# Kernel optimization log

Hardware: AMD Instinct MI355X
Metric: run time of the kernel (lower is better)

## Reference

```python
import jax, jax.numpy as jnp
from jax import lax
import numpy as np

ALPHA = 0.5; EPS = 1e-6; RANK_PAIRS = 100
W_MEAN = 0.5; W_STD = 0.5
L_STAT = 1.0; L_RANK = 1.0; L_SMOOTH = 1.0
LABELS = np.array([5, 8, 13], dtype=np.int32)
TGT_CV = np.array([0.077, 0.227, 0.348], dtype=np.float32)


def _erode(mask_f):
    # torch: 1 - max_pool2d(1-x, k=3, pad=1); implicit -inf padding means
    # out-of-bounds pixels act as foreground -> min-pool with +inf init.
    return lax.reduce_window(mask_f, jnp.inf, lax.min, (3, 3), (1, 1), 'SAME') > 0.5


def _per_region(pred, pix, region, tgt_cv, key):
    # pred, pix: [H,W] float; region: [H,W] bool
    H, W = pred.shape
    HW = H * W
    regf = region.astype(jnp.float32)
    e1 = _erode(regf)
    e2 = _erode(e1.astype(jnp.float32))  # erode(region, iterations=2)
    core1 = jnp.where(jnp.sum(e1) < 2, region, e1)
    core2 = jnp.where(jnp.sum(e2) < 3, core1, e2)
    n_reg = jnp.sum(region)

    # ---- std (coefficient-of-variation) term on core2
    c2 = core2.astype(jnp.float32)
    n2 = jnp.sum(c2)
    n2s = jnp.maximum(n2, 1.0)
    mu = jnp.sum(pred * c2) / n2s
    var = jnp.sum(c2 * (pred - mu) ** 2) / n2s  # unbiased=False
    cv = jnp.sqrt(var) / (jnp.abs(mu) + EPS)
    std_val = jnp.abs(cv - tgt_cv)
    std_valid = (n_reg >= 3) & (n2 >= 3)

    # ---- pairwise rank term on core1 (sampled-pair path; realistic regions
    # always have n > full_pair_threshold=20)
    c1f = core1.reshape(-1).astype(jnp.float32)
    n1 = jnp.sum(c1f)
    p = jnp.where(n1 > 0, c1f / jnp.maximum(n1, 1.0), 1.0 / HW)
    k1, k2 = jax.random.split(key)
    ii = jax.random.choice(k1, HW, (RANK_PAIRS,), replace=True, p=p)
    jj = jax.random.choice(k2, HW, (RANK_PAIRS,), replace=True, p=p)
    pf = pred.reshape(-1)
    xf = pix.reshape(-1)
    s = jnp.sign(xf[ii] - xf[jj])
    pv = ((ii != jj) & (s != 0)).astype(jnp.float32)
    hinge = jax.nn.relu(-(pf[ii] - pf[jj]) * s)
    npv = jnp.sum(pv)
    rank_val = jnp.sum(hinge * pv) / jnp.maximum(npv, 1.0)
    rank_valid = (n_reg >= 2) & (n1 >= 2) & (npv > 0)

    # ---- smoothness term on core2
    dx = jnp.abs(pred[:, 1:] - pred[:, :-1])
    mx = (core2[:, 1:] & core2[:, :-1]).astype(jnp.float32)
    dy = jnp.abs(pred[1:, :] - pred[:-1, :])
    my = (core2[1:, :] & core2[:-1, :]).astype(jnp.float32)
    cx = jnp.sum(mx); cy = jnp.sum(my)
    mean_x = jnp.sum(dx * mx) / jnp.maximum(cx, 1.0)
    mean_y = jnp.sum(dy * my) / jnp.maximum(cy, 1.0)
    hx = (cx > 0).astype(jnp.float32); hy = (cy > 0).astype(jnp.float32)
    npres = hx + hy
    smooth_val = (mean_x * hx + mean_y * hy) / jnp.maximum(npres, 1.0)
    smooth_valid = (n_reg >= 3) & (n2 >= 3) & (npres > 0)

    return std_val, std_valid, rank_val, rank_valid, smooth_val, smooth_valid


def _masked_mean(v, valid):
    vf = valid.astype(jnp.float32)
    c = jnp.sum(vf)
    return jnp.where(c > 0, jnp.sum(v * vf) / jnp.maximum(c, 1.0), 0.0)


def _forward(pred, target, lab14, img1, img2):
    B, _, H, W = pred.shape
    p2 = pred[:, 0]
    lab = lab14[:, 0]
    t1 = img1[:, 0]
    t2 = img2[:, 0]
    pix = (1.0 - ALPHA) * (1.0 - t1) + ALPHA * t2  # pixel_map
    loss_mean = jnp.mean(jnp.abs(pred - target))

    labels = jnp.asarray(LABELS)
    regions = lab[:, None, :, :] == labels[None, :, None, None]  # [B,3,H,W]
    R = regions.reshape(B * 3, H, W)
    P = jnp.broadcast_to(p2[:, None], (B, 3, H, W)).reshape(B * 3, H, W)
    X = jnp.broadcast_to(pix[:, None], (B, 3, H, W)).reshape(B * 3, H, W)
    T = jnp.tile(jnp.asarray(TGT_CV), B)  # [B*3], label-minor matches reshape
    keys = jax.random.split(jax.random.key(42), B * 3)

    sv, svd, rv, rvd, mv, mvd = jax.vmap(_per_region)(P, X, R, T, keys)
    loss_std = _masked_mean(sv, svd)
    loss_rank = _masked_mean(rv, rvd)
    loss_smooth = _masked_mean(mv, mvd)

    loss_stat = W_MEAN * loss_mean + W_STD * loss_std
    return L_STAT * loss_stat + L_RANK * loss_rank + L_SMOOTH * loss_smooth


def setup_inputs() -> dict:
    key = jax.random.key(0)
    k1, k2, k3, k4, k5 = jax.random.split(key, 5)
    B, H, W = 16, 512, 512
    pred = jax.random.normal(k1, (B, 1, H, W), dtype=jnp.float32)
    target = jax.random.normal(k2, (B, 1, H, W), dtype=jnp.float32)
    lab14 = jax.random.randint(k3, (B, 1, H, W), 0, 15, dtype=jnp.int32)
    img1 = jax.random.uniform(k4, (B, 1, H, W), dtype=jnp.float32)
    img2 = jax.random.uniform(k5, (B, 1, H, W), dtype=jnp.float32)
    return {"pred": pred, "target": target, "lab14": lab14, "img1": img1, "img2": img2}


def reference(pred, target, lab14, img1, img2):
    return _forward(pred, target, lab14, img1, img2)
```

## Files before the change

### kernel.cpp

```cpp
#include <hip/hip_runtime.h>

#define BB 16
#define HH 512
#define WW 512
#define BH 8
#define NR (BH+5)
#define NBANDS (HH/BH)
#define NREG 48
#define HWTOT (HH*WW)

#define OFF_SUMABS 4608
#define OFF_COUNTS 4616
#define OFF_RANKV  6344
#define OFF_RANKD  6536
#define OFF_MREG   8192
#define MASKBYTES  (48LL*512*8*8)
#define OFF_ME1    (OFF_MREG + MASKBYTES)

__device__ __forceinline__ unsigned int hashu(unsigned int x) {
  x ^= x >> 16; x *= 0x7feb352dU; x ^= x >> 15; x *= 0x846ca68bU; x ^= x >> 16;
  return x;
}

__global__ __launch_bounds__(256) void pass1_kernel(
    const float* __restrict__ pred, const float* __restrict__ target,
    const int* __restrict__ lab,
    double* __restrict__ sums, double* __restrict__ sumAbs,
    int* __restrict__ counts,
    unsigned long long* __restrict__ mRegG, unsigned long long* __restrict__ mE1G)
{
  __shared__ unsigned long long REG[3][NR][8];
  __shared__ unsigned long long Hh [3][NR][8];
  __shared__ unsigned long long E1v[3][NR][8];
  __shared__ unsigned long long E1H[3][NR][8];
  __shared__ unsigned long long E2v[3][NR][8];
  __shared__ int   Lc[27];
  __shared__ float RED[4][37];

  const int t    = threadIdx.x;
  const int lane = t & 63;
  const int wv   = t >> 6;
  const int r0   = blockIdx.x * BH;
  const int b    = blockIdx.y;
  const int R    = r0 - 3;

  if (t < 27) Lc[t] = 0;

  for (int lr = 0; lr < NR; ++lr) {
    int gy = R + lr;
    int l1 = -1, l2 = -1;
    if ((unsigned)gy < (unsigned)HH) {
      const int* lp = lab + ((size_t)b*HH + gy)*WW;
      l1 = lp[t]; l2 = lp[t+256];
    }
    unsigned long long m1, m2;
    m1 = __ballot(l1 == 5);  m2 = __ballot(l2 == 5);
    if (lane == 0) { REG[0][lr][wv] = m1; REG[0][lr][wv+4] = m2; }
    m1 = __ballot(l1 == 8);  m2 = __ballot(l2 == 8);
    if (lane == 0) { REG[1][lr][wv] = m1; REG[1][lr][wv+4] = m2; }
    m1 = __ballot(l1 == 13); m2 = __ballot(l2 == 13);
    if (lane == 0) { REG[2][lr][wv] = m1; REG[2][lr][wv+4] = m2; }
  }
  __syncthreads();

  for (int task = t; task < 3*NR*8; task += 256) {
    int w = task & 7, q = task >> 3;
    int lr = q % NR, li = q / NR;
    unsigned long long m  = REG[li][lr][w];
    unsigned long long lm = (m << 1) | (w ? (REG[li][lr][w-1] >> 63) : 1ULL);
    unsigned long long rm = (m >> 1) | ((w < 7) ? (REG[li][lr][w+1] << 63) : (1ULL << 63));
    Hh[li][lr][w] = m & lm & rm;
  }
  __syncthreads();
  for (int task = t; task < 3*(NR-2)*8; task += 256) {
    int w = task & 7, q = task >> 3;
    int lr = q % (NR-2) + 1, li = q / (NR-2);
    int gy = R + lr;
    unsigned long long v = Hh[li][lr][w];
    if (gy - 1 >= 0) v &= Hh[li][lr-1][w];
    if (gy + 1 < HH) v &= Hh[li][lr+1][w];
    E1v[li][lr][w] = v;
  }
  __syncthreads();
  for (int task = t; task < 3*(NR-2)*8; task += 256) {
    int w = task & 7, q = task >> 3;
    int lr = q % (NR-2) + 1, li = q / (NR-2);
    unsigned long long m  = E1v[li][lr][w];
    unsigned long long lm = (m << 1) | (w ? (E1v[li][lr][w-1] >> 63) : 1ULL);
    unsigned long long rm = (m >> 1) | ((w < 7) ? (E1v[li][lr][w+1] << 63) : (1ULL << 63));
    E1H[li][lr][w] = m & lm & rm;
  }
  __syncthreads();
  for (int task = t; task < 3*(NR-4)*8; task += 256) {
    int w = task & 7, q = task >> 3;
    int lr = q % (NR-4) + 2, li = q / (NR-4);
    int gy = R + lr;
    unsigned long long v = E1H[li][lr][w];
    if (gy - 1 >= 0) v &= E1H[li][lr-1][w];
    if (gy + 1 < HH) v &= E1H[li][lr+1][w];
    E2v[li][lr][w] = v;
  }
  __syncthreads();

  for (int task = t; task < 3*BH*8; task += 256) {
    int w   = task & 7;
    int row = (task >> 3) % BH;
    int li  = task / (BH*8);
    int gy  = r0 + row;
    int lr  = row + 3;
    size_t base = (((size_t)(b*3 + li))*HH + gy)*8 + w;
    mRegG[base] = REG[li][lr][w];
    mE1G[base]  = E1v[li][lr][w];
  }

  for (int task = t; task < 9*64; task += 256) {
    int idx = task & 63, combo = task >> 6;
    int li = combo / 3, m = combo % 3;
    int row = idx >> 3, w = idx & 7;
    int lr = row + 3, gy = r0 + row;
    const unsigned long long (*M)[8] = (m == 0) ? REG[li] : ((m == 1) ? E1v[li] : E2v[li]);
    unsigned long long mm = M[lr][w];
    int c = __popcll(mm);
    unsigned long long nx = (w < 7) ? M[lr][w+1] : 0ULL;
    int cx = __popcll(mm & ((mm >> 1) | (nx << 63)));
    int cy = (gy > 0) ? __popcll(mm & M[lr-1][w]) : 0;
    atomicAdd(&Lc[combo*3 + 0], c);
    atomicAdd(&Lc[combo*3 + 1], cx);
    atomicAdd(&Lc[combo*3 + 2], cy);
  }

  float aP[9]  = {};
  float aP2[9] = {};
  float aDX[9] = {};
  float aDY[9] = {};
  float aAbs = 0.f;

  const int w1 = wv;
  const int b1 = lane;

  float p1_prev = 0.f, p2_prev = 0.f;
  if (r0 > 0) {
    const float* pr = pred + ((size_t)b*HH + (r0-1))*WW;
    p1_prev = pr[t]; p2_prev = pr[t+256];
  }

  __syncthreads();

  if (t < 27) {
    int combo = t / 3, stat = t % 3;
    int li = combo / 3, m = combo % 3;
    atomicAdd(counts + (b*3 + li)*9 + stat*3 + m, Lc[t]);
  }

  unsigned int ub1 = 0, ub2 = 0;
  #pragma unroll
  for (int li = 0; li < 3; ++li) {
    #pragma unroll
    for (int m = 0; m < 3; ++m) {
      const int cb = li*3 + m;
      const unsigned long long (*M)[8] = (m == 0) ? REG[li] : ((m == 1) ? E1v[li] : E2v[li]);
      ub1 |= (((unsigned int)(M[2][w1]   >> b1)) & 1u) << cb;
      ub2 |= (((unsigned int)(M[2][w1+4] >> b1)) & 1u) << cb;
    }
  }

  const bool hasR2 = (t < 255);
  for (int row = 0; row < BH; ++row) {
    int gy = r0 + row;
    int lr = row + 3;
    const float* prow = pred   + ((size_t)b*HH + gy)*WW;
    const float* trow = target + ((size_t)b*HH + gy)*WW;
    float p1 = prow[t], p2 = prow[t+256];
    float pr1 = prow[t+1];
    float pr2 = hasR2 ? prow[t+257] : 0.f;
    float tg1 = trow[t], tg2 = trow[t+256];
    aAbs += fabsf(p1 - tg1) + fabsf(p2 - tg2);
    float d1 = fabsf(pr1 - p1);
    float d2 = fabsf(pr2 - p2);
    float v1 = fabsf(p1 - p1_prev);
    float v2 = fabsf(p2 - p2_prev);
    float p1s = p1*p1, p2s = p2*p2;
    const bool hasUp = (gy > 0);
    unsigned int nb1 = 0, nb2 = 0;
    #pragma unroll
    for (int li = 0; li < 3; ++li) {
      #pragma unroll
      for (int m = 0; m < 3; ++m) {
        const int cb = li*3 + m;
        const unsigned long long (*M)[8] = (m == 0) ? REG[li] : ((m == 1) ? E1v[li] : E2v[li]);
        unsigned long long cur1 = M[lr][w1];
        unsigned long long cur2 = M[lr][w1+4];
        unsigned int c1 = (unsigned int)(cur1 >> b1) & 1u;
        unsigned int c2 = (unsigned int)(cur2 >> b1) & 1u;
        unsigned int r1, r2;
        if (b1 < 63) {
          r1 = (unsigned int)(cur1 >> (b1+1)) & 1u;
          r2 = (unsigned int)(cur2 >> (b1+1)) & 1u;
        } else {
          r1 = (unsigned int)M[lr][w1+1] & 1u;
          r2 = (w1 < 3) ? ((unsigned int)M[lr][w1+5] & 1u) : 0u;
        }
        unsigned int u1 = hasUp ? ((ub1 >> cb) & 1u) : 0u;
        unsigned int u2 = hasUp ? ((ub2 >> cb) & 1u) : 0u;
        if (c1) { aP[cb] += p1; aP2[cb] += p1s; }
        if (c2) { aP[cb] += p2; aP2[cb] += p2s; }
        if (c1 & r1) aDX[cb] += d1;
        if (hasR2 & (bool)(c2 & r2)) aDX[cb] += d2;
        if (c1 & u1) aDY[cb] += v1;
        if (c2 & u2) aDY[cb] += v2;
        nb1 |= c1 << cb;
        nb2 |= c2 << cb;
      }
    }
    ub1 = nb1; ub2 = nb2;
    p1_prev = p1; p2_prev = p2;
  }

  #pragma unroll
  for (int cb = 0; cb < 9; ++cb) {
    float s0 = aP[cb], s1 = aP2[cb], s2 = aDX[cb], s3 = aDY[cb];
    for (int off = 32; off; off >>= 1) {
      s0 += __shfl_down(s0, off);
      s1 += __shfl_down(s1, off);
      s2 += __shfl_down(s2, off);
      s3 += __shfl_down(s3, off);
    }
    if (lane == 0) {
      RED[wv][0*9 + cb] = s0;
      RED[wv][1*9 + cb] = s1;
      RED[wv][2*9 + cb] = s2;
      RED[wv][3*9 + cb] = s3;
    }
  }
  {
    float va = aAbs;
    for (int off = 32; off; off >>= 1) va += __shfl_down(va, off);
    if (lane == 0) RED[wv][36] = va;
  }
  __syncthreads();
  if (t < 37) {
    float s = RED[0][t] + RED[1][t] + RED[2][t] + RED[3][t];
    if (t < 36) {
      int stat = t / 9, cb = t % 9;
      int li = cb / 3, m = cb % 3;
      atomicAdd(sums + (size_t)(b*3 + li)*12 + stat*3 + m, (double)s);
    } else {
      atomicAdd(sumAbs, (double)s);
    }
  }
}

__global__ __launch_bounds__(256) void pass2_kernel(
    const float* __restrict__ pred, const float* __restrict__ img1,
    const float* __restrict__ img2,
    const unsigned long long* __restrict__ mRegG,
    const unsigned long long* __restrict__ mE1G,
    const int* __restrict__ counts,
    float* __restrict__ rankval, int* __restrict__ rankvalid)
{
  const int r = blockIdx.x;
  const int b = r / 3;
  const int t = threadIdx.x;
  __shared__ int rowc[HH];
  __shared__ int pre[HH];
  __shared__ int grpPre[64];
  __shared__ int idxArr[200];
  __shared__ float redH[100];
  __shared__ int   redP[100];

  int n_reg = counts[r*9 + 0];
  int n_e1  = counts[r*9 + 1];
  int useE1 = (n_e1 >= 2);
  int n1 = useE1 ? n_e1 : n_reg;
  if (!(n_reg >= 2 && n1 >= 2)) {
    if (t == 0) { rankval[r] = 0.f; rankvalid[r] = 0; }
    return;
  }
  const unsigned long long* M = (useE1 ? mE1G : mRegG) + (size_t)r*HH*8;

  {
    int row = t*2;
    int c0 = 0, c1 = 0;
    #pragma unroll
    for (int w = 0; w < 8; ++w) c0 += __popcll(M[row*8 + w]);
    #pragma unroll
    for (int w = 0; w < 8; ++w) c1 += __popcll(M[(row+1)*8 + w]);
    rowc[row] = c0; rowc[row+1] = c1;
  }
  __syncthreads();
  if (t < 64) {
    int base = t*8, s = 0;
    #pragma unroll
    for (int k = 0; k < 8; ++k) s += rowc[base + k];
    int v = s;
    for (int off = 1; off < 64; off <<= 1) {
      int o = __shfl_up(v, off);
      if (t >= off) v += o;
    }
    grpPre[t] = v - s;
  }
  __syncthreads();
  if (t < 64) {
    int s = grpPre[t];
    int base = t*8;
    #pragma unroll
    for (int k = 0; k < 8; ++k) { pre[base + k] = s; s += rowc[base + k]; }
  }
  __syncthreads();

  if (t < 200) {
    unsigned int h = hashu(0x9e3779b9u + (unsigned)(r*200 + t));
    float u = (float)(h >> 8) * (1.0f / 16777216.0f);
    int k = (int)(u * (float)n1);
    if (k >= n1) k = n1 - 1;
    if (k < 0) k = 0;
    int lo = 0, hi = HH;
    while (hi - lo > 1) { int mid = (lo + hi) >> 1; if (pre[mid] <= k) lo = mid; else hi = mid; }
    int row = lo;
    int local = k - pre[row];
    int idx = 0;
    #pragma unroll
    for (int w = 0; w < 8; ++w) {
      unsigned long long mm = M[row*8 + w];
      int c = __popcll(mm);
      if (local < c) {
        for (int i = 0; i < local; ++i) mm &= mm - 1;
        idx = row*WW + w*64 + __builtin_ctzll(mm);
        local = 1 << 20;
      } else {
        local -= c;
      }
    }
    idxArr[t] = idx;
  }
  __syncthreads();

  if (t < 100) {
    int ii = idxArr[t], jj = idxArr[t+100];
    size_t base = (size_t)b * HWTOT;
    float pi = pred[base+ii], pj = pred[base+jj];
    float xi = 0.5f*(1.f - img1[base+ii]) + 0.5f*img2[base+ii];
    float xj = 0.5f*(1.f - img1[base+jj]) + 0.5f*img2[base+jj];
    float s = (xi > xj) ? 1.f : ((xi < xj) ? -1.f : 0.f);
    int pv = (ii != jj) && (s != 0.f);
    float hinge = fmaxf(0.f, -(pi - pj)*s);
    redH[t] = pv ? hinge : 0.f;
    redP[t] = pv;
  }
  __syncthreads();
  if (t == 0) {
    float sh = 0.f; int sp = 0;
    for (int i = 0; i < 100; ++i) { sh += redH[i]; sp += redP[i]; }
    rankval[r]   = sh / (float)(sp > 0 ? sp : 1);
    rankvalid[r] = (sp > 0) ? 1 : 0;
  }
}

__global__ __launch_bounds__(64) void pass3_kernel(
    const double* __restrict__ sums, const double* __restrict__ sumAbs,
    const int* __restrict__ counts,
    const float* __restrict__ rankval, const int* __restrict__ rankvalid,
    float* __restrict__ out)
{
  const int t = threadIdx.x;
  __shared__ double svv[NREG]; __shared__ int svd[NREG];
  __shared__ double smv[NREG]; __shared__ int smd[NREG];
  if (t < NREG) {
    int li = t % 3;
    const int* C = counts + t*9;
    const double* S = sums + (size_t)t*12;
    int n_reg = C[0], n_e1 = C[1], n_e2 = C[2];
    int m1 = (n_e1 < 2) ? 0 : 1;
    int m2 = (n_e2 < 3) ? m1 : 2;
    int n2 = C[m2];
    double n2s = (double)(n2 > 1 ? n2 : 1);
    double mu  = S[m2] / n2s;
    double var = S[3+m2] / n2s - mu*mu;
    if (var < 0.0) var = 0.0;
    double cv = sqrt(var) / (fabs(mu) + 1e-6);
    double tcv = (li == 0) ? 0.077 : ((li == 1) ? 0.227 : 0.348);
    svv[t] = fabs(cv - tcv);
    svd[t] = (n_reg >= 3 && n2 >= 3);
    int cx = C[3+m2], cy = C[6+m2];
    double mean_x = S[6+m2] / (double)(cx > 1 ? cx : 1);
    double mean_y = S[9+m2] / (double)(cy > 1 ? cy : 1);
    int hx = (cx > 0), hy = (cy > 0);
    int npres = hx + hy;
    smv[t] = (mean_x*hx + mean_y*hy) / (double)(npres > 1 ? npres : 1);
    smd[t] = (n_reg >= 3 && n2 >= 3 && npres > 0);
  }
  __syncthreads();
  if (t == 0) {
    double s_std = 0, s_sm = 0, s_rk = 0;
    int c_std = 0, c_sm = 0, c_rk = 0;
    for (int i = 0; i < NREG; ++i) {
      if (svd[i])       { s_std += svv[i];     c_std++; }
      if (smd[i])       { s_sm  += smv[i];     c_sm++;  }
      if (rankvalid[i]) { s_rk  += rankval[i]; c_rk++;  }
    }
    double loss_std = c_std ? s_std / c_std : 0.0;
    double loss_sm  = c_sm  ? s_sm  / c_sm  : 0.0;
    double loss_rk  = c_rk  ? s_rk  / c_rk  : 0.0;
    double loss_mean = sumAbs[0] / (double)((long long)BB * HWTOT);
    double total = 0.5*loss_mean + 0.5*loss_std + loss_rk + loss_sm;
    out[0] = (float)total;
  }
}

extern "C" void kernel_launch(void* const* d_in, const int* in_sizes, int n_in,
                              void* d_out, int out_size, void* d_ws, size_t ws_size,
                              hipStream_t stream) {
  const float* pred   = (const float*)d_in[0];
  const float* target = (const float*)d_in[1];
  const int*   lab    = (const int*)d_in[2];
  const float* img1   = (const float*)d_in[3];
  const float* img2   = (const float*)d_in[4];
  float* out = (float*)d_out;
  char* ws = (char*)d_ws;

  double* sums    = (double*)ws;
  double* sumAbs  = (double*)(ws + OFF_SUMABS);
  int*    counts  = (int*)(ws + OFF_COUNTS);
  float*  rankval = (float*)(ws + OFF_RANKV);
  int*    rankvld = (int*)(ws + OFF_RANKD);
  unsigned long long* mReg = (unsigned long long*)(ws + OFF_MREG);
  unsigned long long* mE1  = (unsigned long long*)(ws + OFF_ME1);

  hipMemsetAsync(ws, 0, 8192, stream);

  dim3 g1(NBANDS, BB);
  pass1_kernel<<<g1, 256, 0, stream>>>(pred, target, lab, sums, sumAbs, counts, mReg, mE1);
  pass2_kernel<<<NREG, 256, 0, stream>>>(pred, img1, img2, mReg, mE1, counts, rankval, rankvld);
  pass3_kernel<<<1, 64, 0, stream>>>(sums, sumAbs, counts, rankval, rankvld, out);
}
```

Baseline: 160.1 us.

## Column-bitmask erosion in pass1, precomputed row counts, fuse final reduction into pass2

Pass1 now uses 512 threads, one per column, and a 16-row band. Each thread keeps a 21-bit vertical bitmask per label, and erosion becomes shift-ANDs plus neighbor exchange through shared memory, replacing the multi-stage shared-memory erosion of 64-bit row words. Pass1 also writes per-row popcounts, so pass2 no longer recomputes them from the masks. Pass2 reduces the rank hinge with warp shuffles. The old pass3 is folded into pass2 through a last-block atomic counter, which removes one kernel launch. The trade-offs are more registers per thread, 16-bit packed counters that could overflow in principle, and grid-level completion detection that relies on atomics and fences.

```diff
diff --git a/kernel.cpp b/kernel.cpp
--- a/kernel.cpp
+++ b/kernel.cpp
@@ -3,17 +3,21 @@
 #define BB 16
 #define HH 512
 #define WW 512
-#define BH 8
+#define BH 16
 #define NR (BH+5)
 #define NBANDS (HH/BH)
 #define NREG 48
 #define HWTOT (HH*WW)
+#define MASK21 0x1FFFFFu
 
 #define OFF_SUMABS 4608
 #define OFF_COUNTS 4616
 #define OFF_RANKV  6344
 #define OFF_RANKD  6536
-#define OFF_MREG   8192
+#define OFF_CTR    6728
+#define OFF_ROWCR  8192
+#define OFF_ROWCE  (OFF_ROWCR + 48*512*4)
+#define OFF_MREG   (OFF_ROWCE + 48*512*4)
 #define MASKBYTES  (48LL*512*8*8)
 #define OFF_ME1    (OFF_MREG + MASKBYTES)
 
@@ -22,198 +26,172 @@
   return x;
 }
 
-__global__ __launch_bounds__(256) void pass1_kernel(
+__global__ __launch_bounds__(512, 4) void pass1_kernel(
     const float* __restrict__ pred, const float* __restrict__ target,
     const int* __restrict__ lab,
     double* __restrict__ sums, double* __restrict__ sumAbs,
     int* __restrict__ counts,
-    unsigned long long* __restrict__ mRegG, unsigned long long* __restrict__ mE1G)
+    unsigned long long* __restrict__ mRegG, unsigned long long* __restrict__ mE1G,
+    int* __restrict__ rowcR, int* __restrict__ rowcE)
 {
-  __shared__ unsigned long long REG[3][NR][8];
-  __shared__ unsigned long long Hh [3][NR][8];
-  __shared__ unsigned long long E1v[3][NR][8];
-  __shared__ unsigned long long E1H[3][NR][8];
-  __shared__ unsigned long long E2v[3][NR][8];
-  __shared__ int   Lc[27];
-  __shared__ float RED[4][37];
+  __shared__ unsigned long long XCH[514];
+  __shared__ unsigned long long NB0[512];
+  __shared__ unsigned long long NB1[512];
+  __shared__ unsigned int      NB2[512];
+  __shared__ int   RC[96];
+  __shared__ float RED[8][37];
+  __shared__ unsigned int CNT[8][14];
 
   const int t    = threadIdx.x;
   const int lane = t & 63;
   const int wv   = t >> 6;
+  const int c    = t;
   const int r0   = blockIdx.x * BH;
   const int b    = blockIdx.y;
   const int R    = r0 - 3;
 
-  if (t < 27) Lc[t] = 0;
-
+  if (t < 96) RC[t] = 0;
+
+  unsigned int OOR = 0;
+  {
+    int topClip = -R;
+    if (topClip > 0) OOR |= (1u << topClip) - 1u;
+    int botStart = HH - R;
+    if (botStart < NR) OOR |= (~0u << botStart) & ((1u << NR) - 1u);
+  }
+
+  unsigned int colm0 = 0, colm1 = 0, colm2 = 0;
   for (int lr = 0; lr < NR; ++lr) {
     int gy = R + lr;
-    int l1 = -1, l2 = -1;
     if ((unsigned)gy < (unsigned)HH) {
-      const int* lp = lab + ((size_t)b*HH + gy)*WW;
-      l1 = lp[t]; l2 = lp[t+256];
-    }
-    unsigned long long m1, m2;
-    m1 = __ballot(l1 == 5);  m2 = __ballot(l2 == 5);
-    if (lane == 0) { REG[0][lr][wv] = m1; REG[0][lr][wv+4] = m2; }
-    m1 = __ballot(l1 == 8);  m2 = __ballot(l2 == 8);
-    if (lane == 0) { REG[1][lr][wv] = m1; REG[1][lr][wv+4] = m2; }
-    m1 = __ballot(l1 == 13); m2 = __ballot(l2 == 13);
-    if (lane == 0) { REG[2][lr][wv] = m1; REG[2][lr][wv+4] = m2; }
-  }
-  __syncthreads();
-
-  for (int task = t; task < 3*NR*8; task += 256) {
-    int w = task & 7, q = task >> 3;
-    int lr = q % NR, li = q / NR;
-    unsigned long long m  = REG[li][lr][w];
-    unsigned long long lm = (m << 1) | (w ? (REG[li][lr][w-1] >> 63) : 1ULL);
-    unsigned long long rm = (m >> 1) | ((w < 7) ? (REG[li][lr][w+1] << 63) : (1ULL << 63));
-    Hh[li][lr][w] = m & lm & rm;
-  }
-  __syncthreads();
-  for (int task = t; task < 3*(NR-2)*8; task += 256) {
-    int w = task & 7, q = task >> 3;
-    int lr = q % (NR-2) + 1, li = q / (NR-2);
-    int gy = R + lr;
-    unsigned long long v = Hh[li][lr][w];
-    if (gy - 1 >= 0) v &= Hh[li][lr-1][w];
-    if (gy + 1 < HH) v &= Hh[li][lr+1][w];
-    E1v[li][lr][w] = v;
-  }
-  __syncthreads();
-  for (int task = t; task < 3*(NR-2)*8; task += 256) {
-    int w = task & 7, q = task >> 3;
-    int lr = q % (NR-2) + 1, li = q / (NR-2);
-    unsigned long long m  = E1v[li][lr][w];
-    unsigned long long lm = (m << 1) | (w ? (E1v[li][lr][w-1] >> 63) : 1ULL);
-    unsigned long long rm = (m >> 1) | ((w < 7) ? (E1v[li][lr][w+1] << 63) : (1ULL << 63));
-    E1H[li][lr][w] = m & lm & rm;
-  }
-  __syncthreads();
-  for (int task = t; task < 3*(NR-4)*8; task += 256) {
-    int w = task & 7, q = task >> 3;
-    int lr = q % (NR-4) + 2, li = q / (NR-4);
-    int gy = R + lr;
-    unsigned long long v = E1H[li][lr][w];
-    if (gy - 1 >= 0) v &= E1H[li][lr-1][w];
-    if (gy + 1 < HH) v &= E1H[li][lr+1][w];
-    E2v[li][lr][w] = v;
-  }
-  __syncthreads();
-
-  for (int task = t; task < 3*BH*8; task += 256) {
-    int w   = task & 7;
-    int row = (task >> 3) % BH;
-    int li  = task / (BH*8);
-    int gy  = r0 + row;
-    int lr  = row + 3;
-    size_t base = (((size_t)(b*3 + li))*HH + gy)*8 + w;
-    mRegG[base] = REG[li][lr][w];
-    mE1G[base]  = E1v[li][lr][w];
-  }
-
-  for (int task = t; task < 9*64; task += 256) {
-    int idx = task & 63, combo = task >> 6;
-    int li = combo / 3, m = combo % 3;
-    int row = idx >> 3, w = idx & 7;
-    int lr = row + 3, gy = r0 + row;
-    const unsigned long long (*M)[8] = (m == 0) ? REG[li] : ((m == 1) ? E1v[li] : E2v[li]);
-    unsigned long long mm = M[lr][w];
-    int c = __popcll(mm);
-    unsigned long long nx = (w < 7) ? M[lr][w+1] : 0ULL;
-    int cx = __popcll(mm & ((mm >> 1) | (nx << 63)));
-    int cy = (gy > 0) ? __popcll(mm & M[lr-1][w]) : 0;
-    atomicAdd(&Lc[combo*3 + 0], c);
-    atomicAdd(&Lc[combo*3 + 1], cx);
-    atomicAdd(&Lc[combo*3 + 2], cy);
-  }
-
-  float aP[9]  = {};
-  float aP2[9] = {};
-  float aDX[9] = {};
-  float aDY[9] = {};
-  float aAbs = 0.f;
-
-  const int w1 = wv;
-  const int b1 = lane;
-
-  float p1_prev = 0.f, p2_prev = 0.f;
-  if (r0 > 0) {
-    const float* pr = pred + ((size_t)b*HH + (r0-1))*WW;
-    p1_prev = pr[t]; p2_prev = pr[t+256];
-  }
-
-  __syncthreads();
-
-  if (t < 27) {
-    int combo = t / 3, stat = t % 3;
-    int li = combo / 3, m = combo % 3;
-    atomicAdd(counts + (b*3 + li)*9 + stat*3 + m, Lc[t]);
-  }
-
-  unsigned int ub1 = 0, ub2 = 0;
+      int l = lab[((size_t)b*HH + gy)*WW + c];
+      colm0 |= (l == 5)  ? (1u << lr) : 0u;
+      colm1 |= (l == 8)  ? (1u << lr) : 0u;
+      colm2 |= (l == 13) ? (1u << lr) : 0u;
+    }
+  }
+
+  unsigned long long pk =  (unsigned long long)(colm0 | OOR)
+        | ((unsigned long long)(colm1 | OOR) << 21)
+        | ((unsigned long long)(colm2 | OOR) << 42);
+  XCH[c+1] = pk;
+  if (t == 0) { XCH[0] = ~0ull; XCH[513] = ~0ull; }
+  __syncthreads();
+  unsigned long long hp = pk & XCH[c] & XCH[c+2];
+  unsigned int e1a[3];
   #pragma unroll
   for (int li = 0; li < 3; ++li) {
-    #pragma unroll
-    for (int m = 0; m < 3; ++m) {
-      const int cb = li*3 + m;
-      const unsigned long long (*M)[8] = (m == 0) ? REG[li] : ((m == 1) ? E1v[li] : E2v[li]);
-      ub1 |= (((unsigned int)(M[2][w1]   >> b1)) & 1u) << cb;
-      ub2 |= (((unsigned int)(M[2][w1+4] >> b1)) & 1u) << cb;
-    }
-  }
-
-  const bool hasR2 = (t < 255);
+    unsigned int h = (unsigned int)((hp >> (21*li)) & MASK21);
+    e1a[li] = h & (h >> 1) & (h << 1);
+  }
+  __syncthreads();
+  unsigned long long pk2 =  (unsigned long long)((e1a[0] | OOR) & MASK21)
+        | ((unsigned long long)((e1a[1] | OOR) & MASK21) << 21)
+        | ((unsigned long long)((e1a[2] | OOR) & MASK21) << 42);
+  XCH[c+1] = pk2;
+  __syncthreads();
+  unsigned long long hp2 = pk2 & XCH[c] & XCH[c+2];
+  unsigned int e2a[3];
+  #pragma unroll
+  for (int li = 0; li < 3; ++li) {
+    unsigned int h = (unsigned int)((hp2 >> (21*li)) & MASK21);
+    e2a[li] = h & (h >> 1) & (h << 1);
+  }
+
+  unsigned int mS[9] = { colm0, e1a[0], e2a[0],
+                         colm1, e1a[1], e2a[1],
+                         colm2, e1a[2], e2a[2] };
+
+  {
+    unsigned long long p0 = 0, p1 = 0;
+    #pragma unroll
+    for (int cb = 0; cb < 4; ++cb) p0 |= (unsigned long long)((mS[cb] >> 3) & 0xFFFFu) << (cb*16);
+    #pragma unroll
+    for (int cb = 4; cb < 8; ++cb) p1 |= (unsigned long long)((mS[cb] >> 3) & 0xFFFFu) << ((cb-4)*16);
+    NB0[c] = p0; NB1[c] = p1; NB2[c] = (mS[8] >> 3) & 0xFFFFu;
+  }
+  __syncthreads();
+  unsigned long long nb0 = (c < 511) ? NB0[c+1] : 0ull;
+  unsigned long long nb1 = (c < 511) ? NB1[c+1] : 0ull;
+  unsigned int       nb2 = (c < 511) ? NB2[c+1] : 0u;
+
+  {
+    unsigned int pkc[14];
+    #pragma unroll
+    for (int j = 0; j < 14; ++j) pkc[j] = 0;
+    #pragma unroll
+    for (int cb = 0; cb < 9; ++cb) {
+      unsigned int w16 = (mS[cb] >> 3) & 0xFFFFu;
+      unsigned int nbw;
+      if (cb < 4)      nbw = (unsigned int)(nb0 >> (cb*16)) & 0xFFFFu;
+      else if (cb < 8) nbw = (unsigned int)(nb1 >> ((cb-4)*16)) & 0xFFFFu;
+      else             nbw = nb2 & 0xFFFFu;
+      unsigned int mcl = mS[cb] & ~OOR;
+      unsigned int q   = mcl & (mcl << 1);
+      unsigned int cnt = __popc(w16);
+      unsigned int cx  = __popc(w16 & nbw);
+      unsigned int cy  = __popc((q >> 3) & 0xFFFFu);
+      int k0 = cb*3;
+      pkc[(k0  )>>1] |= cnt << (((k0  )&1)*16);
+      pkc[(k0+1)>>1] |= cx  << (((k0+1)&1)*16);
+      pkc[(k0+2)>>1] |= cy  << (((k0+2)&1)*16);
+    }
+    #pragma unroll
+    for (int j = 0; j < 14; ++j) {
+      unsigned int v = pkc[j];
+      for (int off = 32; off; off >>= 1) v += __shfl_down(v, off);
+      if (lane == 0) CNT[wv][j] = v;
+    }
+  }
+
   for (int row = 0; row < BH; ++row) {
-    int gy = r0 + row;
-    int lr = row + 3;
-    const float* prow = pred   + ((size_t)b*HH + gy)*WW;
-    const float* trow = target + ((size_t)b*HH + gy)*WW;
-    float p1 = prow[t], p2 = prow[t+256];
-    float pr1 = prow[t+1];
-    float pr2 = hasR2 ? prow[t+257] : 0.f;
-    float tg1 = trow[t], tg2 = trow[t+256];
-    aAbs += fabsf(p1 - tg1) + fabsf(p2 - tg2);
-    float d1 = fabsf(pr1 - p1);
-    float d2 = fabsf(pr2 - p2);
-    float v1 = fabsf(p1 - p1_prev);
-    float v2 = fabsf(p2 - p2_prev);
-    float p1s = p1*p1, p2s = p2*p2;
-    const bool hasUp = (gy > 0);
-    unsigned int nb1 = 0, nb2 = 0;
+    int lr = row + 3, gy = r0 + row;
     #pragma unroll
     for (int li = 0; li < 3; ++li) {
-      #pragma unroll
-      for (int m = 0; m < 3; ++m) {
-        const int cb = li*3 + m;
-        const unsigned long long (*M)[8] = (m == 0) ? REG[li] : ((m == 1) ? E1v[li] : E2v[li]);
-        unsigned long long cur1 = M[lr][w1];
-        unsigned long long cur2 = M[lr][w1+4];
-        unsigned int c1 = (unsigned int)(cur1 >> b1) & 1u;
-        unsigned int c2 = (unsigned int)(cur2 >> b1) & 1u;
-        unsigned int r1, r2;
-        if (b1 < 63) {
-          r1 = (unsigned int)(cur1 >> (b1+1)) & 1u;
-          r2 = (unsigned int)(cur2 >> (b1+1)) & 1u;
-        } else {
-          r1 = (unsigned int)M[lr][w1+1] & 1u;
-          r2 = (w1 < 3) ? ((unsigned int)M[lr][w1+5] & 1u) : 0u;
-        }
-        unsigned int u1 = hasUp ? ((ub1 >> cb) & 1u) : 0u;
-        unsigned int u2 = hasUp ? ((ub2 >> cb) & 1u) : 0u;
-        if (c1) { aP[cb] += p1; aP2[cb] += p1s; }
-        if (c2) { aP[cb] += p2; aP2[cb] += p2s; }
-        if (c1 & r1) aDX[cb] += d1;
-        if (hasR2 & (bool)(c2 & r2)) aDX[cb] += d2;
-        if (c1 & u1) aDY[cb] += v1;
-        if (c2 & u2) aDY[cb] += v2;
-        nb1 |= c1 << cb;
-        nb2 |= c2 << cb;
+      unsigned long long wR = __ballot((mS[li*3]   >> lr) & 1u);
+      unsigned long long wE = __ballot((mS[li*3+1] >> lr) & 1u);
+      if (lane == 0) {
+        size_t base = (((size_t)(b*3 + li))*HH + gy)*8 + wv;
+        mRegG[base] = wR; mE1G[base] = wE;
+        atomicAdd(&RC[     li*BH + row], (int)__popcll(wR));
+        atomicAdd(&RC[48 + li*BH + row], (int)__popcll(wE));
       }
     }
-    ub1 = nb1; ub2 = nb2;
-    p1_prev = p1; p2_prev = p2;
+  }
+
+  float aP[9] = {}, aP2[9] = {}, aDX[9] = {}, aDY[9] = {};
+  float aAbs = 0.f;
+  const float* pB = pred   + (size_t)b*HH*WW;
+  const float* tB = target + (size_t)b*HH*WW;
+  float p_prev = (r0 > 0) ? pB[(size_t)(r0-1)*WW + c] : 0.f;
+  const int cR = (c < 511) ? c + 1 : c;
+
+  #pragma unroll
+  for (int row = 0; row < BH; ++row) {
+    const int lr = row + 3, gy = r0 + row;
+    const float* prow = pB + (size_t)gy*WW;
+    float p  = prow[c];
+    float pr = prow[cR];
+    float tg = tB[(size_t)gy*WW + c];
+    aAbs += fabsf(p - tg);
+    float d = fabsf(pr - p);
+    float v = (gy > 0) ? fabsf(p - p_prev) : 0.f;
+    #pragma unroll
+    for (int cb = 0; cb < 9; ++cb) {
+      unsigned int cur = mS[cb];
+      unsigned int c1 = (cur >> lr) & 1u;
+      unsigned int u1 = (cur >> (lr-1)) & 1u;
+      unsigned int r1;
+      if (cb < 4)      r1 = (unsigned int)(nb0 >> (cb*16 + row)) & 1u;
+      else if (cb < 8) r1 = (unsigned int)(nb1 >> ((cb-4)*16 + row)) & 1u;
+      else             r1 = (nb2 >> row) & 1u;
+      float f = c1 ? p : 0.f;
+      aP[cb]  += f;
+      aP2[cb]  = fmaf(f, p, aP2[cb]);
+      aDX[cb] += (c1 & r1) ? d : 0.f;
+      aDY[cb] += (c1 & u1) ? v : 0.f;
+    }
+    p_prev = p;
   }
 
   #pragma unroll
@@ -226,10 +204,8 @@
       s3 += __shfl_down(s3, off);
     }
     if (lane == 0) {
-      RED[wv][0*9 + cb] = s0;
-      RED[wv][1*9 + cb] = s1;
-      RED[wv][2*9 + cb] = s2;
-      RED[wv][3*9 + cb] = s3;
+      RED[wv][0*9 + cb] = s0; RED[wv][1*9 + cb] = s1;
+      RED[wv][2*9 + cb] = s2; RED[wv][3*9 + cb] = s3;
     }
   }
   {
@@ -238,15 +214,38 @@
     if (lane == 0) RED[wv][36] = va;
   }
   __syncthreads();
+
   if (t < 37) {
-    float s = RED[0][t] + RED[1][t] + RED[2][t] + RED[3][t];
+    float s = 0.f;
+    #pragma unroll
+    for (int w = 0; w < 8; ++w) s += RED[w][t];
     if (t < 36) {
-      int stat = t / 9, cb = t % 9;
-      int li = cb / 3, m = cb % 3;
+      int stat = t / 9, cb = t % 9, li = cb / 3, m = cb % 3;
       atomicAdd(sums + (size_t)(b*3 + li)*12 + stat*3 + m, (double)s);
     } else {
       atomicAdd(sumAbs, (double)s);
     }
+  }
+  if (t < 14) {
+    unsigned int s = 0;
+    #pragma unroll
+    for (int w = 0; w < 8; ++w) s += CNT[w][t];
+    int k0 = t*2;
+    #pragma unroll
+    for (int h = 0; h < 2; ++h) {
+      int k = k0 + h;
+      if (k < 27) {
+        unsigned int val = (s >> (h*16)) & 0xFFFFu;
+        int cb = k / 3, stat = k % 3, li = cb / 3, m = cb % 3;
+        atomicAdd(counts + (b*3 + li)*9 + stat*3 + m, (int)val);
+      }
+    }
+  }
+  if (t < 96) {
+    int type = t / 48, rem = t % 48;
+    int li = rem / BH, row = rem % BH, gy = r0 + row;
+    int* dst = type ? rowcE : rowcR;
+    dst[((size_t)(b*3 + li))*HH + gy] = RC[t];
   }
 }
 
@@ -255,155 +254,166 @@
     const float* __restrict__ img2,
     const unsigned long long* __restrict__ mRegG,
     const unsigned long long* __restrict__ mE1G,
+    const int* __restrict__ rowcR, const int* __restrict__ rowcE,
     const int* __restrict__ counts,
-    float* __restrict__ rankval, int* __restrict__ rankvalid)
+    const double* __restrict__ sums, const double* __restrict__ sumAbs,
+    float* __restrict__ rankval, int* __restrict__ rankvalid,
+    int* __restrict__ ctr, float* __restrict__ out)
 {
   const int r = blockIdx.x;
   const int b = r / 3;
   const int t = threadIdx.x;
+  const int lane = t & 63;
+  const int wv   = t >> 6;
   __shared__ int rowc[HH];
   __shared__ int pre[HH];
   __shared__ int grpPre[64];
   __shared__ int idxArr[200];
-  __shared__ float redH[100];
-  __shared__ int   redP[100];
+  __shared__ float redH[4];
+  __shared__ int   redP[4];
+  __shared__ int lastFlag;
+  __shared__ double svvS[NREG], smvS[NREG];
+  __shared__ int svdS[NREG], smdS[NREG];
+  __shared__ float rkvS[NREG];
+  __shared__ int   rkdS[NREG];
 
   int n_reg = counts[r*9 + 0];
   int n_e1  = counts[r*9 + 1];
   int useE1 = (n_e1 >= 2);
   int n1 = useE1 ? n_e1 : n_reg;
-  if (!(n_reg >= 2 && n1 >= 2)) {
-    if (t == 0) { rankval[r] = 0.f; rankvalid[r] = 0; }
-    return;
-  }
-  const unsigned long long* M = (useE1 ? mE1G : mRegG) + (size_t)r*HH*8;
-
-  {
-    int row = t*2;
-    int c0 = 0, c1 = 0;
-    #pragma unroll
-    for (int w = 0; w < 8; ++w) c0 += __popcll(M[row*8 + w]);
-    #pragma unroll
-    for (int w = 0; w < 8; ++w) c1 += __popcll(M[(row+1)*8 + w]);
-    rowc[row] = c0; rowc[row+1] = c1;
-  }
-  __syncthreads();
-  if (t < 64) {
-    int base = t*8, s = 0;
-    #pragma unroll
-    for (int k = 0; k < 8; ++k) s += rowc[base + k];
-    int v = s;
-    for (int off = 1; off < 64; off <<= 1) {
-      int o = __shfl_up(v, off);
-      if (t >= off) v += o;
-    }
-    grpPre[t] = v - s;
-  }
-  __syncthreads();
-  if (t < 64) {
-    int s = grpPre[t];
-    int base = t*8;
-    #pragma unroll
-    for (int k = 0; k < 8; ++k) { pre[base + k] = s; s += rowc[base + k]; }
-  }
-  __syncthreads();
-
-  if (t < 200) {
-    unsigned int h = hashu(0x9e3779b9u + (unsigned)(r*200 + t));
-    float u = (float)(h >> 8) * (1.0f / 16777216.0f);
-    int k = (int)(u * (float)n1);
-    if (k >= n1) k = n1 - 1;
-    if (k < 0) k = 0;
-    int lo = 0, hi = HH;
-    while (hi - lo > 1) { int mid = (lo + hi) >> 1; if (pre[mid] <= k) lo = mid; else hi = mid; }
-    int row = lo;
-    int local = k - pre[row];
-    int idx = 0;
-    #pragma unroll
-    for (int w = 0; w < 8; ++w) {
-      unsigned long long mm = M[row*8 + w];
-      int c = __popcll(mm);
-      if (local < c) {
-        for (int i = 0; i < local; ++i) mm &= mm - 1;
-        idx = row*WW + w*64 + __builtin_ctzll(mm);
-        local = 1 << 20;
-      } else {
-        local -= c;
+  bool doRank = (n_reg >= 2 && n1 >= 2);
+  float rv = 0.f; int rvd = 0;
+
+  if (doRank) {
+    const int* rc = (useE1 ? rowcE : rowcR) + (size_t)r*HH;
+    { int2 vv = ((const int2*)rc)[t]; rowc[2*t] = vv.x; rowc[2*t+1] = vv.y; }
+    __syncthreads();
+    if (t < 64) {
+      int base = t*8, s = 0;
+      #pragma unroll
+      for (int k = 0; k < 8; ++k) s += rowc[base + k];
+      int v = s;
+      for (int off = 1; off < 64; off <<= 1) {
+        int o = __shfl_up(v, off);
+        if (t >= off) v += o;
       }
-    }
-    idxArr[t] = idx;
-  }
-  __syncthreads();
-
-  if (t < 100) {
-    int ii = idxArr[t], jj = idxArr[t+100];
-    size_t base = (size_t)b * HWTOT;
-    float pi = pred[base+ii], pj = pred[base+jj];
-    float xi = 0.5f*(1.f - img1[base+ii]) + 0.5f*img2[base+ii];
-    float xj = 0.5f*(1.f - img1[base+jj]) + 0.5f*img2[base+jj];
-    float s = (xi > xj) ? 1.f : ((xi < xj) ? -1.f : 0.f);
-    int pv = (ii != jj) && (s != 0.f);
-    float hinge = fmaxf(0.f, -(pi - pj)*s);
-    redH[t] = pv ? hinge : 0.f;
-    redP[t] = pv;
-  }
-  __syncthreads();
+      grpPre[t] = v - s;
+    }
+    __syncthreads();
+    if (t < 64) {
+      int s = grpPre[t], base = t*8;
+      #pragma unroll
+      for (int k = 0; k < 8; ++k) { pre[base + k] = s; s += rowc[base + k]; }
+    }
+    __syncthreads();
+
+    const unsigned long long* M = (useE1 ? mE1G : mRegG) + (size_t)r*HH*8;
+    if (t < 200) {
+      unsigned int h = hashu(0x9e3779b9u + (unsigned)(r*200 + t));
+      float u = (float)(h >> 8) * (1.0f / 16777216.0f);
+      int k = (int)(u * (float)n1);
+      if (k >= n1) k = n1 - 1;
+      if (k < 0) k = 0;
+      int lo = 0, hi = HH;
+      while (hi - lo > 1) { int mid = (lo + hi) >> 1; if (pre[mid] <= k) lo = mid; else hi = mid; }
+      int row = lo;
+      int local = k - pre[row];
+      int idx = 0;
+      #pragma unroll
+      for (int w = 0; w < 8; ++w) {
+        unsigned long long mm = M[row*8 + w];
+        int cc = __popcll(mm);
+        if (local < cc) {
+          for (int i = 0; i < local; ++i) mm &= mm - 1;
+          idx = row*WW + w*64 + __builtin_ctzll(mm);
+          local = 1 << 20;
+        } else {
+          local -= cc;
+        }
+      }
+      idxArr[t] = idx;
+    }
+    __syncthreads();
+
+    float hv = 0.f; int pv = 0;
+    if (t < 100) {
+      int ii = idxArr[t], jj = idxArr[t+100];
+      size_t base = (size_t)b * HWTOT;
+      float pi = pred[base+ii], pj = pred[base+jj];
+      float xi = 0.5f*(1.f - img1[base+ii]) + 0.5f*img2[base+ii];
+      float xj = 0.5f*(1.f - img1[base+jj]) + 0.5f*img2[base+jj];
+      float s = (xi > xj) ? 1.f : ((xi < xj) ? -1.f : 0.f);
+      pv = (ii != jj) && (s != 0.f);
+      float hinge = fmaxf(0.f, -(pi - pj)*s);
+      hv = pv ? hinge : 0.f;
+    }
+    for (int off = 32; off; off >>= 1) {
+      hv += __shfl_down(hv, off);
+      pv += __shfl_down(pv, off);
+    }
+    if (lane == 0) { redH[wv] = hv; redP[wv] = pv; }
+    __syncthreads();
+    if (t == 0) {
+      float sh = redH[0] + redH[1] + redH[2] + redH[3];
+      int   sp = redP[0] + redP[1] + redP[2] + redP[3];
+      rv  = sh / (float)(sp > 0 ? sp : 1);
+      rvd = (sp > 0) ? 1 : 0;
+    }
+  }
+
   if (t == 0) {
-    float sh = 0.f; int sp = 0;
-    for (int i = 0; i < 100; ++i) { sh += redH[i]; sp += redP[i]; }
-    rankval[r]   = sh / (float)(sp > 0 ? sp : 1);
-    rankvalid[r] = (sp > 0) ? 1 : 0;
-  }
-}
-
-__global__ __launch_bounds__(64) void pass3_kernel(
-    const double* __restrict__ sums, const double* __restrict__ sumAbs,
-    const int* __restrict__ counts,
-    const float* __restrict__ rankval, const int* __restrict__ rankvalid,
-    float* __restrict__ out)
-{
-  const int t = threadIdx.x;
-  __shared__ double svv[NREG]; __shared__ int svd[NREG];
-  __shared__ double smv[NREG]; __shared__ int smd[NREG];
-  if (t < NREG) {
-    int li = t % 3;
-    const int* C = counts + t*9;
-    const double* S = sums + (size_t)t*12;
-    int n_reg = C[0], n_e1 = C[1], n_e2 = C[2];
-    int m1 = (n_e1 < 2) ? 0 : 1;
-    int m2 = (n_e2 < 3) ? m1 : 2;
-    int n2 = C[m2];
-    double n2s = (double)(n2 > 1 ? n2 : 1);
-    double mu  = S[m2] / n2s;
-    double var = S[3+m2] / n2s - mu*mu;
-    if (var < 0.0) var = 0.0;
-    double cv = sqrt(var) / (fabs(mu) + 1e-6);
-    double tcv = (li == 0) ? 0.077 : ((li == 1) ? 0.227 : 0.348);
-    svv[t] = fabs(cv - tcv);
-    svd[t] = (n_reg >= 3 && n2 >= 3);
-    int cx = C[3+m2], cy = C[6+m2];
-    double mean_x = S[6+m2] / (double)(cx > 1 ? cx : 1);
-    double mean_y = S[9+m2] / (double)(cy > 1 ? cy : 1);
-    int hx = (cx > 0), hy = (cy > 0);
-    int npres = hx + hy;
-    smv[t] = (mean_x*hx + mean_y*hy) / (double)(npres > 1 ? npres : 1);
-    smd[t] = (n_reg >= 3 && n2 >= 3 && npres > 0);
-  }
-  __syncthreads();
-  if (t == 0) {
-    double s_std = 0, s_sm = 0, s_rk = 0;
-    int c_std = 0, c_sm = 0, c_rk = 0;
-    for (int i = 0; i < NREG; ++i) {
-      if (svd[i])       { s_std += svv[i];     c_std++; }
-      if (smd[i])       { s_sm  += smv[i];     c_sm++;  }
-      if (rankvalid[i]) { s_rk  += rankval[i]; c_rk++;  }
-    }
-    double loss_std = c_std ? s_std / c_std : 0.0;
-    double loss_sm  = c_sm  ? s_sm  / c_sm  : 0.0;
-    double loss_rk  = c_rk  ? s_rk  / c_rk  : 0.0;
-    double loss_mean = sumAbs[0] / (double)((long long)BB * HWTOT);
-    double total = 0.5*loss_mean + 0.5*loss_std + loss_rk + loss_sm;
-    out[0] = (float)total;
+    atomicExch(&rankval[r], rv);
+    atomicExch(&rankvalid[r], rvd);
+    __threadfence();
+    int old = atomicAdd(ctr, 1);
+    lastFlag = (old == NREG - 1);
+  }
+  __syncthreads();
+
+  if (lastFlag) {
+    __threadfence();
+    if (t < NREG) {
+      int li = t % 3;
+      const int* C = counts + t*9;
+      const double* S = sums + (size_t)t*12;
+      int nr = C[0], ne1 = C[1], ne2 = C[2];
+      int m1 = (ne1 < 2) ? 0 : 1;
+      int m2 = (ne2 < 3) ? m1 : 2;
+      int n2 = C[m2];
+      double n2s = (double)(n2 > 1 ? n2 : 1);
+      double mu  = S[m2] / n2s;
+      double var = S[3+m2] / n2s - mu*mu;
+      if (var < 0.0) var = 0.0;
+      double cv = sqrt(var) / (fabs(mu) + 1e-6);
+      double tcv = (li == 0) ? 0.077 : ((li == 1) ? 0.227 : 0.348);
+      svvS[t] = fabs(cv - tcv);
+      svdS[t] = (nr >= 3 && n2 >= 3);
+      int cx = C[3+m2], cy = C[6+m2];
+      double mean_x = S[6+m2] / (double)(cx > 1 ? cx : 1);
+      double mean_y = S[9+m2] / (double)(cy > 1 ? cy : 1);
+      int hx = (cx > 0), hy = (cy > 0);
+      int npres = hx + hy;
+      smvS[t] = (mean_x*hx + mean_y*hy) / (double)(npres > 1 ? npres : 1);
+      smdS[t] = (nr >= 3 && n2 >= 3 && npres > 0);
+      rkvS[t] = rankval[t];
+      rkdS[t] = rankvalid[t];
+    }
+    __syncthreads();
+    if (t == 0) {
+      double s_std = 0, s_sm = 0, s_rk = 0;
+      int c_std = 0, c_sm = 0, c_rk = 0;
+      for (int i = 0; i < NREG; ++i) {
+        if (svdS[i]) { s_std += svvS[i]; c_std++; }
+        if (smdS[i]) { s_sm  += smvS[i]; c_sm++;  }
+        if (rkdS[i]) { s_rk  += rkvS[i]; c_rk++;  }
+      }
+      double loss_std = c_std ? s_std / c_std : 0.0;
+      double loss_sm  = c_sm  ? s_sm  / c_sm  : 0.0;
+      double loss_rk  = c_rk  ? s_rk  / c_rk  : 0.0;
+      double loss_mean = sumAbs[0] / (double)((long long)BB * HWTOT);
+      double total = 0.5*loss_mean + 0.5*loss_std + loss_rk + loss_sm;
+      out[0] = (float)total;
+    }
   }
 }
 
@@ -423,13 +433,17 @@
   int*    counts  = (int*)(ws + OFF_COUNTS);
   float*  rankval = (float*)(ws + OFF_RANKV);
   int*    rankvld = (int*)(ws + OFF_RANKD);
+  int*    ctr     = (int*)(ws + OFF_CTR);
+  int*    rowcR   = (int*)(ws + OFF_ROWCR);
+  int*    rowcE   = (int*)(ws + OFF_ROWCE);
   unsigned long long* mReg = (unsigned long long*)(ws + OFF_MREG);
   unsigned long long* mE1  = (unsigned long long*)(ws + OFF_ME1);
 
   hipMemsetAsync(ws, 0, 8192, stream);
 
   dim3 g1(NBANDS, BB);
-  pass1_kernel<<<g1, 256, 0, stream>>>(pred, target, lab, sums, sumAbs, counts, mReg, mE1);
-  pass2_kernel<<<NREG, 256, 0, stream>>>(pred, img1, img2, mReg, mE1, counts, rankval, rankvld);
-  pass3_kernel<<<1, 64, 0, stream>>>(sums, sumAbs, counts, rankval, rankvld, out);
+  pass1_kernel<<<g1, 512, 0, stream>>>(pred, target, lab, sums, sumAbs, counts,
+                                       mReg, mE1, rowcR, rowcE);
+  pass2_kernel<<<NREG, 256, 0, stream>>>(pred, img1, img2, mReg, mE1, rowcR, rowcE,
+                                         counts, sums, sumAbs, rankval, rankvld, ctr, out);
 }
```

Result: no change. 158.0 us (-1.3%).
